# Kernel optimization log

Hardware: AMD Instinct MI355X
Metric: run time of the kernel (lower is better)

Reference implementation:

```python
import jax, jax.numpy as jnp
import numpy as np

N = 100000   # num_nodes
E = 1000000  # num_edges
H = 64       # hidden_dim
M = 64       # msg_dim
C = 16       # num_classes


def setup_inputs() -> dict:
    key = jax.random.key(0)
    ks = jax.random.split(key, 16)
    s = 1.0 / np.sqrt(H)
    inp = {
        "features": jax.random.normal(ks[0], (N, H), jnp.float32),
        "src": jax.random.randint(ks[1], (E,), 0, N, dtype=jnp.int32),
        "dst": jax.random.randint(ks[2], (E,), 0, N, dtype=jnp.int32),
        "edge_types": jax.random.randint(ks[3], (E,), 0, 2, dtype=jnp.int32) == 1,
        # per-edge-type message linears (edge_matrix[0] for type==True, [1] for type==False)
        "W0": jax.random.uniform(ks[4], (M, H), jnp.float32, -s, s),
        "b0": jax.random.uniform(ks[5], (M,), jnp.float32, -s, s),
        "W1": jax.random.uniform(ks[6], (M, H), jnp.float32, -s, s),
        "b1": jax.random.uniform(ks[7], (M,), jnp.float32, -s, s),
        # GRU (single layer, single step): gates order [r, z, n] as in torch
        "W_ih": jax.random.uniform(ks[8], (3 * H, M), jnp.float32, -s, s),
        "W_hh": jax.random.uniform(ks[9], (3 * H, H), jnp.float32, -s, s),
        "b_ih": jax.random.uniform(ks[10], (3 * H,), jnp.float32, -s, s),
        "b_hh": jax.random.uniform(ks[11], (3 * H,), jnp.float32, -s, s),
        # output classifier
        "W_out": jax.random.uniform(ks[12], (C, H), jnp.float32, -s, s),
        "b_out": jax.random.uniform(ks[13], (C,), jnp.float32, -s, s),
    }
    return inp


def reference(features, src, dst, edge_types,
              W0, b0, W1, b1, W_ih, W_hh, b_ih, b_hh, W_out, b_out):
    # gather source-node features per edge: [E, H]
    x = features[src]
    # tiny per-edge-type linear; select by edge type
    m0 = x @ W0.T + b0            # type True  -> edge_matrix[0]
    m1 = x @ W1.T + b1            # type False -> edge_matrix[1]
    msg = jnp.where(edge_types[:, None], m0, m1)  # [E, M]
    # scatter-add messages into node buffer (zero-initialized accumulator)
    agg = jax.ops.segment_sum(msg, dst, num_segments=N)  # [N, M]
    # single GRU step: input=agg, hidden=features
    gi = agg @ W_ih.T + b_ih       # [N, 3H]
    gh = features @ W_hh.T + b_hh  # [N, 3H]
    i_r, i_z, i_n = jnp.split(gi, 3, axis=-1)
    h_r, h_z, h_n = jnp.split(gh, 3, axis=-1)
    r = jax.nn.sigmoid(i_r + h_r)
    z = jax.nn.sigmoid(i_z + h_z)
    n = jnp.tanh(i_n + r * h_n)
    h = (1.0 - z) * n + z * features  # [N, H]
    # output classifier
    return h @ W_out.T + b_out        # [N, C]
```

## Files before the change

kernel.cpp:

```cpp
#include <hip/hip_runtime.h>


typedef __bf16 bf16x8 __attribute__((ext_vector_type(8)));
typedef float  f32x4  __attribute__((ext_vector_type(4)));
typedef int    i32x4  __attribute__((ext_vector_type(4)));

#define MFMA16 __builtin_amdgcn_mfma_f32_16x16x32_bf16
#define NN   100000
#define EE   1000000
#define BB   782
#define NPB  128
#define ECAP 1600
#define DCAP 48
#define CSTRD 49
#define NB   245
#define NWL  24576

__device__ __forceinline__ float sigmoidf_(float x) {
    return 1.0f / (1.0f + __expf(-x));
}

__device__ __forceinline__ bf16x8 ldw(const __bf16* w, int e) {
    int bo = e * 2;
    bo ^= ((bo >> 7) & 7) << 4;
    return *(const bf16x8*)((const char*)w + bo);
}

__global__ __launch_bounds__(256) void k_init(const unsigned char* __restrict__ et,
                                              const float* __restrict__ feat,
                                              const int* __restrict__ dst,
                                              const float* __restrict__ w0,
                                              const float* __restrict__ w1,
                                              const float* __restrict__ wih,
                                              const float* __restrict__ whh,
                                              const float* __restrict__ wout,
                                              __bf16* __restrict__ featb,
                                              __bf16* __restrict__ wb,
                                              int* __restrict__ hist,
                                              int* __restrict__ flag) {
    int b = blockIdx.x, tid = threadIdx.x;
    if (b == 0) {
        __shared__ int sdet[4];
        const i32x4* p = (const i32x4*)et + tid * 16;
        unsigned acc = 0;
#pragma unroll
        for (int j = 0; j < 16; j++) {
            i32x4 w = p[j];
            acc |= (unsigned)(w[0] | w[1] | w[2] | w[3]) & 0xffffff00u;
        }
        unsigned long long m = __ballot(acc != 0);
        if ((tid & 63) == 0) sdet[tid >> 6] = (m != 0ULL);
        __syncthreads();
        if (tid == 0) *flag = sdet[0] | sdet[1] | sdet[2] | sdet[3];
        return;
    }
    if (b < 133) {
        int i = (b - 1) * 256 + tid;
        float v;
        if      (i < 4096)  v = w0[i];
        else if (i < 8192)  v = w1[i - 4096];
        else if (i < 20480) v = wih[i - 8192];
        else if (i < 32768) v = whh[i - 20480];
        else                v = wout[i - 32768];
        wb[i] = (__bf16)v;
        return;
    }
    if (b >= 6383) {
        __shared__ int cnt[BB];
        int hb = b - 6383;
        for (int i = tid; i < BB; i += 256) cnt[i] = 0;
        __syncthreads();
        long e0 = (long)hb * 4096 + tid * 16;
#pragma unroll
        for (int g = 0; g < 2; g++) {
            long e = e0 + g * 8;
            if (e < EE) {
                i32x4 d0 = *(const i32x4*)(dst + e);
                i32x4 d1 = *(const i32x4*)(dst + e + 4);
#pragma unroll
                for (int j = 0; j < 4; j++) atomicAdd(&cnt[d0[j] >> 7], 1);
#pragma unroll
                for (int j = 0; j < 4; j++) atomicAdd(&cnt[d1[j] >> 7], 1);
            }
        }
        __syncthreads();
        for (int i = tid; i < BB; i += 256) hist[hb * BB + i] = cnt[i];
        return;
    }
    long i = ((long)(b - 133) * 256 + tid) * 4;
    if (i >= (long)NN * 64) return;
    f32x4 v = *(const f32x4*)(feat + i);
    union { __bf16 e[4]; unsigned long long u; } o;
#pragma unroll
    for (int j = 0; j < 4; j++) o.e[j] = (__bf16)v[j];
    *(unsigned long long*)(featb + i) = o.u;
}

__global__ __launch_bounds__(256) void k_s2(const int* __restrict__ hist,
                                            int* __restrict__ blockBase,
                                            int* __restrict__ bucketCnt) {
    int b = blockIdx.x * 4 + (threadIdx.x >> 6);
    int lane = threadIdx.x & 63;
    if (b >= BB) return;
    int carry = 0;
    for (int c = 0; c < 4; c++) {
        int blk = c * 64 + lane;
        int v = (blk < NB) ? hist[blk * BB + b] : 0;
        int x = v;
#pragma unroll
        for (int off = 1; off < 64; off <<= 1) {
            int y = __shfl_up(x, off, 64);
            if (lane >= off) x += y;
        }
        if (blk < NB) blockBase[blk * BB + b] = x - v + carry;
        carry += __shfl(x, 63, 64);
    }
    if (lane == 0) bucketCnt[b] = carry;
}

__global__ __launch_bounds__(512) void k_s3(const int* __restrict__ src,
                                            const int* __restrict__ dst,
                                            const unsigned char* __restrict__ etype,
                                            const int* __restrict__ flag,
                                            const int* __restrict__ blockBase,
                                            int* __restrict__ region) {
    __shared__ int cur[BB];
    int blk = blockIdx.x, tid = threadIdx.x;
    for (int i = tid; i < BB; i += 512) cur[i] = blockBase[blk * BB + i];
    __syncthreads();
    long e0 = (long)blk * 4096 + tid * 8;
    if (e0 >= EE) return;
    i32x4 s0 = *(const i32x4*)(src + e0);
    i32x4 s1 = *(const i32x4*)(src + e0 + 4);
    i32x4 d0 = *(const i32x4*)(dst + e0);
    i32x4 d1 = *(const i32x4*)(dst + e0 + 4);
    int t[8];
    if (*flag) {
        unsigned long long w = *(const unsigned long long*)(etype + e0);
#pragma unroll
        for (int j = 0; j < 8; j++) t[j] = (int)((w >> (8 * j)) & 0xff);
    } else {
        i32x4 w0 = *(const i32x4*)((const int*)etype + e0);
        i32x4 w1 = *(const i32x4*)((const int*)etype + e0 + 4);
#pragma unroll
        for (int j = 0; j < 4; j++) { t[j] = w0[j]; t[4 + j] = w1[j]; }
    }
    int dd[8] = {d0[0], d0[1], d0[2], d0[3], d1[0], d1[1], d1[2], d1[3]};
    int ss[8] = {s0[0], s0[1], s0[2], s0[3], s1[0], s1[1], s1[2], s1[3]};
#pragma unroll
    for (int j = 0; j < 8; j++) {
        int b  = dd[j] >> 7;
        int nl = dd[j] & 127;
        int r  = atomicAdd(&cur[b], 1);
        if (r < ECAP)
            region[b * ECAP + r] = (nl << 18) | ((t[j] ? 1 : 0) << 17) | ss[j];
    }
}

__global__ __launch_bounds__(512) void k_g(const __bf16* __restrict__ featb,
                                           const int* __restrict__ region,
                                           const int* __restrict__ bucketCnt,
                                           __bf16* __restrict__ s1b,
                                           __bf16* __restrict__ s0b,
                                           int* __restrict__ cc) {
    __shared__ int ncnt[NPB];
    __shared__ int csr[NPB * CSTRD];
    int b = blockIdx.x, tid = threadIdx.x;
    int cntE = min(bucketCnt[b], ECAP);
    if (tid < NPB) ncnt[tid] = 0;
    __syncthreads();
    const int* reg = region + b * ECAP;
    for (int i = tid; i < cntE; i += 512) {
        int rec = reg[i];
        int nl = rec >> 18;
        int r = atomicAdd(&ncnt[nl], 1);
        if (r < DCAP) csr[nl * CSTRD + r] = rec & 0x3ffff;
    }
    __syncthreads();

    int lane = tid & 63, wave = tid >> 6;
    int L = lane & 15, q = lane >> 4;
    int nl = wave * 16 + L;
    int n = b * NPB + nl;
    int cnt = (n < NN) ? min(ncnt[nl], DCAP) : 0;
    const int* eb = &csr[nl * CSTRD];

    float sA[16], s1[16];
#pragma unroll
    for (int j = 0; j < 16; j++) { sA[j] = 0.f; s1[j] = 0.f; }
    int c1 = 0;
    int i = 0;
    for (; i + 2 <= cnt; i += 2) {
        int ea = eb[i], ebn = eb[i + 1];
        const __bf16* rowa = featb + (long)(ea & 0x1ffff) * 64;
        const __bf16* rowb = featb + (long)(ebn & 0x1ffff) * 64;
        bf16x8 a0 = *(const bf16x8*)(rowa + q * 8);
        bf16x8 a1 = *(const bf16x8*)(rowa + 32 + q * 8);
        bf16x8 b0v = *(const bf16x8*)(rowb + q * 8);
        bf16x8 b1v = *(const bf16x8*)(rowb + 32 + q * 8);
        int ta = (ea >> 17) & 1, tb = (ebn >> 17) & 1;
        c1 += ta + tb;
        float fa = (float)ta, fb = (float)tb;
#pragma unroll
        for (int j = 0; j < 8; j++) {
            float va = (float)a0[j], wa = (float)a1[j];
            float vb = (float)b0v[j], wb2 = (float)b1v[j];
            sA[j]     += va + vb;
            sA[8 + j] += wa + wb2;
            s1[j]     += fa * va + fb * vb;
            s1[8 + j] += fa * wa + fb * wb2;
        }
    }
    if (i < cnt) {
        int ea = eb[i];
        const __bf16* rowa = featb + (long)(ea & 0x1ffff) * 64;
        bf16x8 a0 = *(const bf16x8*)(rowa + q * 8);
        bf16x8 a1 = *(const bf16x8*)(rowa + 32 + q * 8);
        int ta = (ea >> 17) & 1;
        c1 += ta;
        float fa = (float)ta;
#pragma unroll
        for (int j = 0; j < 8; j++) {
            float va = (float)a0[j], wa = (float)a1[j];
            sA[j] += va;          sA[8 + j] += wa;
            s1[j] += fa * va;     s1[8 + j] += fa * wa;
        }
    }
    if (n >= NN) return;
    union { bf16x8 v; __bf16 e[8]; } u;
#pragma unroll
    for (int ch = 0; ch < 2; ch++) {
#pragma unroll
        for (int j = 0; j < 8; j++) u.e[j] = (__bf16)s1[ch * 8 + j];
        *(bf16x8*)(s1b + (long)n * 64 + ch * 32 + q * 8) = u.v;
#pragma unroll
        for (int j = 0; j < 8; j++) u.e[j] = (__bf16)(sA[ch * 8 + j] - s1[ch * 8 + j]);
        *(bf16x8*)(s0b + (long)n * 64 + ch * 32 + q * 8) = u.v;
    }
    if (q == 0) cc[n] = cnt | (c1 << 16);
}

__global__ __launch_bounds__(512, 4) void k_mm(const __bf16* __restrict__ s1b,
                                               const __bf16* __restrict__ s0b,
                                               const __bf16* __restrict__ featb,
                                               const float* __restrict__ feat,
                                               const int* __restrict__ cc,
                                               const __bf16* __restrict__ wb,
                                               const float* __restrict__ b0,
                                               const float* __restrict__ b1,
                                               const float* __restrict__ bih,
                                               const float* __restrict__ bhh,
                                               const float* __restrict__ bout,
                                               float* __restrict__ out) {
    __shared__ __align__(16) __bf16 wlds[NWL];
    __shared__ __align__(16) __bf16 sHall[8][16 * 80];
    int tid = threadIdx.x, lane = tid & 63, wave = tid >> 6;
    int L = lane & 15, q = lane >> 4;
    int n0 = blockIdx.x * NPB + wave * 16;

    bf16x8 AS1[2], AS0[2], Aft[2];
    float fvv[4][4], fc1[4], fc0[4];
    if (n0 < NN) {
        const __bf16* r1 = s1b + (long)(n0 + L) * 64;
        const __bf16* r0 = s0b + (long)(n0 + L) * 64;
        const __bf16* fr = featb + (long)(n0 + L) * 64;
        AS1[0] = *(const bf16x8*)(r1 + q * 8);  AS1[1] = *(const bf16x8*)(r1 + 32 + q * 8);
        AS0[0] = *(const bf16x8*)(r0 + q * 8);  AS0[1] = *(const bf16x8*)(r0 + 32 + q * 8);
        Aft[0] = *(const bf16x8*)(fr + q * 8);  Aft[1] = *(const bf16x8*)(fr + 32 + q * 8);
#pragma unroll
        for (int nb = 0; nb < 4; nb++)
#pragma unroll
            for (int r = 0; r < 4; r++)
                fvv[nb][r] = feat[(long)(n0 + q * 4 + r) * 64 + nb * 16 + L];
        i32x4 cv = *(const i32x4*)(cc + n0 + q * 4);
#pragma unroll
        for (int r = 0; r < 4; r++) {
            int c1 = cv[r] >> 16, ct = cv[r] & 0xffff;
            fc1[r] = (float)c1; fc0[r] = (float)(ct - c1);
        }
    }

    const __bf16* wsrc = wb + 8192;
    for (int k = tid * 8; k < NWL; k += 512 * 8) {
        bf16x8 v = *(const bf16x8*)(wsrc + k);
        int bo = k * 2;
        int so = bo ^ (((bo >> 7) & 7) << 4);
        *(bf16x8*)((char*)wlds + so) = v;
    }
    __syncthreads();
    if (n0 >= NN) return;

    __bf16* sH = sHall[wave];
    const __bf16* w0b = wb, * w1b = wb + 4096, * woutb = wb + 32768;
    f32x4 zz = {0.f, 0.f, 0.f, 0.f};

#pragma unroll
    for (int nb = 0; nb < 4; nb++) {
        f32x4 acc = zz;
#pragma unroll
        for (int ch = 0; ch < 2; ch++) {
            int off = (nb * 16 + L) * 64 + ch * 32 + q * 8;
            acc = MFMA16(AS1[ch], *(const bf16x8*)(w0b + off), acc, 0, 0, 0);
            acc = MFMA16(AS0[ch], *(const bf16x8*)(w1b + off), acc, 0, 0, 0);
        }
        float bs0 = b0[nb * 16 + L], bs1 = b1[nb * 16 + L];
#pragma unroll
        for (int r = 0; r < 4; r++)
            sH[(q * 4 + r) * 80 + nb * 16 + L] =
                (__bf16)(acc[r] + fc1[r] * bs0 + fc0[r] * bs1);
    }

    bf16x8 Aag[2];
#pragma unroll
    for (int ch = 0; ch < 2; ch++)
        Aag[ch] = *(const bf16x8*)&sH[L * 80 + ch * 32 + q * 8];

#pragma unroll
    for (int nb = 0; nb < 4; nb++) {
        int row = nb * 16 + L;
        f32x4 aR = zz, aZ = zz, aIN = zz, aHN = zz;
#pragma unroll
        for (int ch = 0; ch < 2; ch++) {
            int ko = ch * 32 + q * 8;
            aR  = MFMA16(Aag[ch], ldw(wlds, row * 64 + ko), aR, 0, 0, 0);
            aR  = MFMA16(Aft[ch], ldw(wlds, 12288 + row * 64 + ko), aR, 0, 0, 0);
            aZ  = MFMA16(Aag[ch], ldw(wlds, (64 + row) * 64 + ko), aZ, 0, 0, 0);
            aZ  = MFMA16(Aft[ch], ldw(wlds, 12288 + (64 + row) * 64 + ko), aZ, 0, 0, 0);
            aIN = MFMA16(Aag[ch], ldw(wlds, (128 + row) * 64 + ko), aIN, 0, 0, 0);
            aHN = MFMA16(Aft[ch], ldw(wlds, 12288 + (128 + row) * 64 + ko), aHN, 0, 0, 0);
        }
        int h = row;
        float br  = bih[h] + bhh[h];
        float bz  = bih[64 + h] + bhh[64 + h];
        float bin = bih[128 + h];
        float bhn = bhh[128 + h];
#pragma unroll
        for (int r = 0; r < 4; r++) {
            float rv = sigmoidf_(aR[r] + br);
            float zv = sigmoidf_(aZ[r] + bz);
            float nv = tanhf(aIN[r] + bin + rv * (aHN[r] + bhn));
            float fv = fvv[nb][r];
            sH[(q * 4 + r) * 80 + h] = (__bf16)((1.0f - zv) * nv + zv * fv);
        }
    }

    bf16x8 Ah0 = *(const bf16x8*)&sH[L * 80 + q * 8];
    bf16x8 Ah1 = *(const bf16x8*)&sH[L * 80 + 32 + q * 8];
    bf16x8 Bo0 = *(const bf16x8*)(woutb + L * 64 + q * 8);
    bf16x8 Bo1 = *(const bf16x8*)(woutb + L * 64 + 32 + q * 8);
    f32x4 o = zz;
    o = MFMA16(Ah0, Bo0, o, 0, 0, 0);
    o = MFMA16(Ah1, Bo1, o, 0, 0, 0);
    float bo = bout[L];
#pragma unroll
    for (int r = 0; r < 4; r++)
        out[(long)(n0 + q * 4 + r) * 16 + L] = o[r] + bo;
}

extern "C" void kernel_launch(void* const* d_in, const int* in_sizes, int n_in,
                              void* d_out, int out_size, void* d_ws, size_t ws_size,
                              hipStream_t stream) {
    const float* features = (const float*)d_in[0];
    const int*   src      = (const int*)d_in[1];
    const int*   dst      = (const int*)d_in[2];
    const unsigned char* etype = (const unsigned char*)d_in[3];
    const float* W0   = (const float*)d_in[4];
    const float* b0   = (const float*)d_in[5];
    const float* W1   = (const float*)d_in[6];
    const float* b1   = (const float*)d_in[7];
    const float* Wih  = (const float*)d_in[8];
    const float* Whh  = (const float*)d_in[9];
    const float* bih  = (const float*)d_in[10];
    const float* bhh  = (const float*)d_in[11];
    const float* Wout = (const float*)d_in[12];
    const float* bout = (const float*)d_in[13];
    float* out = (float*)d_out;

    char* ws = (char*)d_ws;
    size_t off = 0;
    __bf16* featb     = (__bf16*)(ws + off); off += (size_t)NN * 64 * 2;
    int*    region    = (int*)(ws + off);    off += (size_t)BB * ECAP * 4;
    int*    hist      = (int*)(ws + off);    off += (size_t)NB * BB * 4;
    int*    blockBase = (int*)(ws + off);    off += (size_t)NB * BB * 4;
    int*    bucketCnt = (int*)(ws + off);    off += (size_t)BB * 4;
    int*    cc        = (int*)(ws + off);    off += (size_t)NN * 4;
    __bf16* s1b       = (__bf16*)(ws + off); off += (size_t)NN * 64 * 2;
    __bf16* s0b       = (__bf16*)(ws + off); off += (size_t)NN * 64 * 2;
    __bf16* wb        = (__bf16*)(ws + off); off += 33792 * 2;
    int*    flag      = (int*)(ws + off);

    k_init<<<6628, 256, 0, stream>>>(etype, features, dst, W0, W1, Wih, Whh,
                                     Wout, featb, wb, hist, flag);
    k_s2<<<(BB + 3) / 4, 256, 0, stream>>>(hist, blockBase, bucketCnt);
    k_s3<<<NB, 512, 0, stream>>>(src, dst, etype, flag, blockBase, region);
    k_g<<<BB, 512, 0, stream>>>(featb, region, bucketCnt, s1b, s0b, cc);
    k_mm<<<BB, 512, 0, stream>>>(s1b, s0b, featb, features, cc, wb,
                                 b0, b1, bih, bhh, bout, out);
}
```

Before: 185.3 us.

## Fuse gather-aggregate kernel with GRU matmul kernel, keeping sums in registers

Merges the per-bucket gather/segment-sum kernel with the message/GRU/classifier MFMA kernel. The aggregated sums and edge counts stay in registers, with counts passed between lanes by shuffles, instead of being written to and reread from global bf16 buffers. The CSR shared buffer is reused as the per-wave scratch for the hidden tile, and weight staging into LDS overlaps the CSR build. This removes one launch and about 25MB of global traffic. In exchange the fused kernel needs more registers and LDS, which may limit occupancy and make gather latency harder to hide.

```diff
diff --git a/kernel.cpp b/kernel.cpp
--- a/kernel.cpp
+++ b/kernel.cpp
@@ -157,15 +157,37 @@
     }
 }
 
-__global__ __launch_bounds__(512) void k_g(const __bf16* __restrict__ featb,
-                                           const int* __restrict__ region,
-                                           const int* __restrict__ bucketCnt,
-                                           __bf16* __restrict__ s1b,
-                                           __bf16* __restrict__ s0b,
-                                           int* __restrict__ cc) {
+__global__ __launch_bounds__(512, 4) void k_gm(const __bf16* __restrict__ featb,
+                                               const int* __restrict__ region,
+                                               const int* __restrict__ bucketCnt,
+                                               const float* __restrict__ feat,
+                                               const __bf16* __restrict__ wb,
+                                               const float* __restrict__ b0,
+                                               const float* __restrict__ b1,
+                                               const float* __restrict__ bih,
+                                               const float* __restrict__ bhh,
+                                               const float* __restrict__ bout,
+                                               float* __restrict__ out) {
+    __shared__ __align__(16) __bf16 wlds[NWL];
+    __shared__ __align__(16) int csr[NPB * CSTRD];
     __shared__ int ncnt[NPB];
-    __shared__ int csr[NPB * CSTRD];
-    int b = blockIdx.x, tid = threadIdx.x;
+    int b = blockIdx.x, tid = threadIdx.x, lane = tid & 63, wave = tid >> 6;
+    int L = lane & 15, q = lane >> 4;
+    int n0 = b * NPB + wave * 16;
+
+    bf16x8 Aft[2];
+    float fvv[4][4];
+    if (n0 < NN) {
+        const __bf16* fr = featb + (long)(n0 + L) * 64;
+        Aft[0] = *(const bf16x8*)(fr + q * 8);
+        Aft[1] = *(const bf16x8*)(fr + 32 + q * 8);
+#pragma unroll
+        for (int nb = 0; nb < 4; nb++)
+#pragma unroll
+            for (int r = 0; r < 4; r++)
+                fvv[nb][r] = feat[(long)(n0 + q * 4 + r) * 64 + nb * 16 + L];
+    }
+
     int cntE = min(bucketCnt[b], ECAP);
     if (tid < NPB) ncnt[tid] = 0;
     __syncthreads();
@@ -176,13 +198,17 @@
         int r = atomicAdd(&ncnt[nl], 1);
         if (r < DCAP) csr[nl * CSTRD + r] = rec & 0x3ffff;
     }
+    const __bf16* wsrc = wb + 8192;
+    for (int k = tid * 8; k < NWL; k += 512 * 8) {
+        bf16x8 v = *(const bf16x8*)(wsrc + k);
+        int bo = k * 2;
+        int so = bo ^ (((bo >> 7) & 7) << 4);
+        *(bf16x8*)((char*)wlds + so) = v;
+    }
     __syncthreads();
 
-    int lane = tid & 63, wave = tid >> 6;
-    int L = lane & 15, q = lane >> 4;
     int nl = wave * 16 + L;
-    int n = b * NPB + nl;
-    int cnt = (n < NN) ? min(ncnt[nl], DCAP) : 0;
+    int cnt = (n0 < NN) ? min(ncnt[nl], DCAP) : 0;
     const int* eb = &csr[nl * CSTRD];
 
     float sA[16], s1[16];
@@ -226,71 +252,31 @@
             s1[j] += fa * va;     s1[8 + j] += fa * wa;
         }
     }
-    if (n >= NN) return;
-    union { bf16x8 v; __bf16 e[8]; } u;
-#pragma unroll
-    for (int ch = 0; ch < 2; ch++) {
-#pragma unroll
-        for (int j = 0; j < 8; j++) u.e[j] = (__bf16)s1[ch * 8 + j];
-        *(bf16x8*)(s1b + (long)n * 64 + ch * 32 + q * 8) = u.v;
-#pragma unroll
-        for (int j = 0; j < 8; j++) u.e[j] = (__bf16)(sA[ch * 8 + j] - s1[ch * 8 + j]);
-        *(bf16x8*)(s0b + (long)n * 64 + ch * 32 + q * 8) = u.v;
-    }
-    if (q == 0) cc[n] = cnt | (c1 << 16);
-}
-
-__global__ __launch_bounds__(512, 4) void k_mm(const __bf16* __restrict__ s1b,
-                                               const __bf16* __restrict__ s0b,
-                                               const __bf16* __restrict__ featb,
-                                               const float* __restrict__ feat,
-                                               const int* __restrict__ cc,
-                                               const __bf16* __restrict__ wb,
-                                               const float* __restrict__ b0,
-                                               const float* __restrict__ b1,
-                                               const float* __restrict__ bih,
-                                               const float* __restrict__ bhh,
-                                               const float* __restrict__ bout,
-                                               float* __restrict__ out) {
-    __shared__ __align__(16) __bf16 wlds[NWL];
-    __shared__ __align__(16) __bf16 sHall[8][16 * 80];
-    int tid = threadIdx.x, lane = tid & 63, wave = tid >> 6;
-    int L = lane & 15, q = lane >> 4;
-    int n0 = blockIdx.x * NPB + wave * 16;
-
-    bf16x8 AS1[2], AS0[2], Aft[2];
-    float fvv[4][4], fc1[4], fc0[4];
-    if (n0 < NN) {
-        const __bf16* r1 = s1b + (long)(n0 + L) * 64;
-        const __bf16* r0 = s0b + (long)(n0 + L) * 64;
-        const __bf16* fr = featb + (long)(n0 + L) * 64;
-        AS1[0] = *(const bf16x8*)(r1 + q * 8);  AS1[1] = *(const bf16x8*)(r1 + 32 + q * 8);
-        AS0[0] = *(const bf16x8*)(r0 + q * 8);  AS0[1] = *(const bf16x8*)(r0 + 32 + q * 8);
-        Aft[0] = *(const bf16x8*)(fr + q * 8);  Aft[1] = *(const bf16x8*)(fr + 32 + q * 8);
-#pragma unroll
-        for (int nb = 0; nb < 4; nb++)
-#pragma unroll
-            for (int r = 0; r < 4; r++)
-                fvv[nb][r] = feat[(long)(n0 + q * 4 + r) * 64 + nb * 16 + L];
-        i32x4 cv = *(const i32x4*)(cc + n0 + q * 4);
-#pragma unroll
-        for (int r = 0; r < 4; r++) {
-            int c1 = cv[r] >> 16, ct = cv[r] & 0xffff;
-            fc1[r] = (float)c1; fc0[r] = (float)(ct - c1);
-        }
-    }
-
-    const __bf16* wsrc = wb + 8192;
-    for (int k = tid * 8; k < NWL; k += 512 * 8) {
-        bf16x8 v = *(const bf16x8*)(wsrc + k);
-        int bo = k * 2;
-        int so = bo ^ (((bo >> 7) & 7) << 4);
-        *(bf16x8*)((char*)wlds + so) = v;
-    }
-    __syncthreads();
     if (n0 >= NN) return;
 
-    __bf16* sH = sHall[wave];
+    bf16x8 AS1[2], AS0[2];
+    {
+        union { bf16x8 v; __bf16 e[8]; } u;
+#pragma unroll
+        for (int ch = 0; ch < 2; ch++) {
+#pragma unroll
+            for (int j = 0; j < 8; j++) u.e[j] = (__bf16)s1[ch * 8 + j];
+            AS1[ch] = u.v;
+#pragma unroll
+            for (int j = 0; j < 8; j++) u.e[j] = (__bf16)(sA[ch * 8 + j] - s1[ch * 8 + j]);
+            AS0[ch] = u.v;
+        }
+    }
+    int ccp = cnt | (c1 << 16);
+    float fc1[4], fc0[4];
+#pragma unroll
+    for (int r = 0; r < 4; r++) {
+        int v = __shfl(ccp, q * 4 + r, 64);
+        int c1v = v >> 16;
+        fc1[r] = (float)c1v; fc0[r] = (float)((v & 0xffff) - c1v);
+    }
+
+    __bf16* sH = (__bf16*)((char*)csr + wave * (16 * CSTRD * 4));
     const __bf16* w0b = wb, * w1b = wb + 4096, * woutb = wb + 32768;
     f32x4 zz = {0.f, 0.f, 0.f, 0.f};
 
@@ -383,9 +369,6 @@
     int*    hist      = (int*)(ws + off);    off += (size_t)NB * BB * 4;
     int*    blockBase = (int*)(ws + off);    off += (size_t)NB * BB * 4;
     int*    bucketCnt = (int*)(ws + off);    off += (size_t)BB * 4;
-    int*    cc        = (int*)(ws + off);    off += (size_t)NN * 4;
-    __bf16* s1b       = (__bf16*)(ws + off); off += (size_t)NN * 64 * 2;
-    __bf16* s0b       = (__bf16*)(ws + off); off += (size_t)NN * 64 * 2;
     __bf16* wb        = (__bf16*)(ws + off); off += 33792 * 2;
     int*    flag      = (int*)(ws + off);
 
@@ -393,7 +376,6 @@
                                      Wout, featb, wb, hist, flag);
     k_s2<<<(BB + 3) / 4, 256, 0, stream>>>(hist, blockBase, bucketCnt);
     k_s3<<<NB, 512, 0, stream>>>(src, dst, etype, flag, blockBase, region);
-    k_g<<<BB, 512, 0, stream>>>(featb, region, bucketCnt, s1b, s0b, cc);
-    k_mm<<<BB, 512, 0, stream>>>(s1b, s0b, featb, features, cc, wb,
+    k_gm<<<BB, 512, 0, stream>>>(featb, region, bucketCnt, features, wb,
                                  b0, b1, bih, bhh, bout, out);
 }
```

Measured after the change: 184.6 us. No clear change (-0.3%).
